# Optimization experiments

Measured on AMD Instinct MI355X. Metric: run time of the kernel, lower is better.

Reference implementation:

```python
import jax, jax.numpy as jnp
import numpy as np


def setup_inputs() -> dict:
    key = jax.random.key(0)
    k1, k2 = jax.random.split(key)
    f = jax.random.normal(k1, (4, 8192, 128), dtype=jnp.float32)
    f_ = jax.random.normal(k2, (4, 8192, 128), dtype=jnp.float32)
    return {"f": f, "f_": f_}


def reference(f, f_):
    # square_distance: [B,N,M] = |f|^2 + |f_|^2 - 2 f.f_
    # dis[b,n,m] = ||f[b,n] - f_[b,m]||^2
    dis = (jnp.sum(f * f, axis=-1)[:, :, None]
           + jnp.sum(f_ * f_, axis=-1)[:, None, :]
           - 2.0 * jnp.einsum('bnc,bmc->bnm', f, f_))
    f2f_ = jnp.min(dis, axis=2)   # [B, N]
    f_2f = jnp.min(dis, axis=1)   # [B, M]
    d = jnp.mean(f2f_, axis=1) + jnp.mean(f_2f, axis=1)  # [B]
    return jnp.mean(d)
```

## Files before the change

kernel.cpp:

```cpp
#include <hip/hip_runtime.h>

#define BATCH 4
#define NPTS 8192
#define DIM 128
#define TOTAL_ROWS (BATCH * NPTS)
#define SLICES 8
#define SLICE_W 1024
#define ITERS 64
#define TILES_PER_B 512
#define TILE_B 2048

typedef __attribute__((ext_vector_type(8))) int   i32x8;
typedef __attribute__((ext_vector_type(4))) float f32x4;

__device__ __forceinline__ unsigned encf(float f) {
  unsigned b = __float_as_uint(f);
  return b ^ ((unsigned)((int)b >> 31) | 0x80000000u);
}
__device__ __forceinline__ float decf(unsigned u) {
  unsigned b = (u & 0x80000000u) ? (u ^ 0x80000000u) : ~u;
  return __uint_as_float(b);
}

__device__ __forceinline__ void pk8(const float4& x, const float4& y,
                                    unsigned& lo, unsigned& hi) {
  lo = __builtin_amdgcn_cvt_pk_fp8_f32(x.x, x.y, 0, 0);
  lo = __builtin_amdgcn_cvt_pk_fp8_f32(x.z, x.w, lo, 1);
  hi = __builtin_amdgcn_cvt_pk_fp8_f32(y.x, y.y, 0, 0);
  hi = __builtin_amdgcn_cvt_pk_fp8_f32(y.z, y.w, hi, 1);
}

__global__ void pack_kernel(const float* __restrict__ f,
                            const float* __restrict__ f_,
                            unsigned char* __restrict__ pkA,
                            unsigned char* __restrict__ pkB,
                            float* __restrict__ fnh,
                            float* __restrict__ gnh,
                            unsigned int* __restrict__ rowmin,
                            unsigned int* __restrict__ colmin) {
  __shared__ float sred[16][17];
  int gb  = blockIdx.x;
  int tl  = threadIdx.x;
  if (tl < 8)        rowmin[gb * 8 + tl]       = 0xFFFFFFFFu;
  else if (tl < 16)  colmin[gb * 8 + (tl - 8)] = 0xFFFFFFFFu;

  const int isA = gb >> 11;
  const float* in = isA ? f : f_;
  unsigned char* pk = isA ? pkA : pkB;
  float* n2h = isA ? fnh : gnh;

  int fl  = tl >> 2;
  int p   = tl & 3;
  int row = fl & 15, kch = fl >> 4;
  int tile = gb & 2047;
  int b = tile >> 9, mtg = tile & 511;
  const float* src = in + (size_t)(b * NPTS + mtg * 16 + row) * DIM + kch * 32 + p * 8;
  float4 x = ((const float4*)src)[0], y = ((const float4*)src)[1];
  unsigned lo, hi;
  pk8(x, y, lo, hi);
  *(uint2*)(pk + (size_t)tile * TILE_B + fl * 32 + p * 8) = make_uint2(lo, hi);
  float s = 0.f;
  s = fmaf(x.x, x.x, s); s = fmaf(x.y, x.y, s);
  s = fmaf(x.z, x.z, s); s = fmaf(x.w, x.w, s);
  s = fmaf(y.x, y.x, s); s = fmaf(y.y, y.y, s);
  s = fmaf(y.z, y.z, s); s = fmaf(y.w, y.w, s);
  sred[row][kch * 4 + p] = s;
  __syncthreads();
  if (tl < 16) {
    float t = 0.f;
    #pragma unroll
    for (int j = 0; j < 16; ++j) t += sred[tl][j];
    n2h[tile * 16 + tl] = -0.5f * t;
  }
}

__global__ __launch_bounds__(256, 4)
void chamfer_mfma_kernel(const unsigned char* __restrict__ pkA,
                         const unsigned char* __restrict__ pkB,
                         const float* __restrict__ fnh,
                         const float* __restrict__ gnh,
                         unsigned int* __restrict__ rowmin,
                         unsigned int* __restrict__ colmin) {
  const int lane = threadIdx.x & 63;
  const int l15  = lane & 15;
  const int q    = lane >> 4;
  const int widx = threadIdx.x >> 6;
  const int loff = lane * 32;

  const int bid   = blockIdx.x;
  const int combo = (bid & 7) * 4 + ((bid >> 3) & 3);
  const int b     = combo >> 3;
  const int slice = combo & 7;
  const int rgrp  = bid >> 5;
  const int r0    = rgrp * 256 + widx * 64;
  const int bN    = b * NPTS;
  const int tile0 = b * TILES_PER_B + slice * ITERS;

  __shared__ unsigned cl[SLICE_W];
  #pragma unroll
  for (int k = 0; k < SLICE_W / 256; ++k)
    cl[threadIdx.x + k * 256] = 0xFFFFFFFFu;
  __syncthreads();

  i32x8 af[4];
  const int atile0 = b * TILES_PER_B + (r0 >> 4);
  #pragma unroll
  for (int t = 0; t < 4; ++t) {
    const unsigned char* ub = pkA + (size_t)(atile0 + t) * TILE_B;
    af[t] = *(const i32x8*)(ub + loff);
  }
  f32x4 h[4];
  #pragma unroll
  for (int t = 0; t < 4; ++t)
    #pragma unroll
    for (int i = 0; i < 4; ++i)
      h[t][i] = fnh[bN + r0 + t * 16 + q * 4 + i];

  float rowmax[4][4];
  #pragma unroll
  for (int t = 0; t < 4; ++t)
    #pragma unroll
    for (int i = 0; i < 4; ++i) rowmax[t][i] = -3.4e38f;

  const unsigned char* pkw = pkB + (size_t)tile0 * TILE_B;
  const float*         gnb = gnh + bN + slice * SLICE_W;

  auto loadB = [&](int mt, i32x8& bf, float& gv) {
    const unsigned char* ub = pkw + (size_t)mt * TILE_B;
    bf = *(const i32x8*)(ub + loff);
    gv = gnb[mt * 16 + l15];
  };

  auto compute = [&](const i32x8& bf, float g2, int mt) {
    f32x4 acc[4];
    __builtin_amdgcn_s_setprio(1);
    #pragma unroll
    for (int t = 0; t < 4; ++t)
      acc[t] = __builtin_amdgcn_mfma_scale_f32_16x16x128_f8f6f4(
          af[t], bf, h[t], 0, 0, 0, 0x7f7f7f7f, 0, 0x7f7f7f7f);
    __builtin_amdgcn_s_setprio(0);

    #pragma unroll
    for (int t = 0; t < 4; ++t)
      #pragma unroll
      for (int i = 0; i < 4; ++i)
        rowmax[t][i] = fmaxf(rowmax[t][i], acc[t][i] + g2);

    float m0 = fmaxf(fmaxf(acc[0][0], acc[0][1]), acc[0][2]);
    float m1 = fmaxf(fmaxf(acc[0][3], acc[1][0]), acc[1][1]);
    float m2 = fmaxf(fmaxf(acc[1][2], acc[1][3]), acc[2][0]);
    float m3 = fmaxf(fmaxf(acc[2][1], acc[2][2]), acc[2][3]);
    float m4 = fmaxf(fmaxf(acc[3][0], acc[3][1]), acc[3][2]);
    float n0 = fmaxf(fmaxf(m0, m1), m2);
    float n1 = fmaxf(fmaxf(m3, m4), acc[3][3]);
    float cmax = fmaxf(n0, n1);
    atomicMin(&cl[mt * 16 + l15], encf(-2.f * cmax));
  };

  i32x8 bA, bB;
  float gA, gB;
  loadB(0, bA, gA);
  for (int mt = 0; mt < ITERS; mt += 2) {
    loadB(mt + 1, bB, gB);
    compute(bA, gA, mt);
    loadB((mt + 2) & (ITERS - 1), bA, gA);
    compute(bB, gB, mt + 1);
  }

  #pragma unroll
  for (int t = 0; t < 4; ++t)
    #pragma unroll
    for (int i = 0; i < 4; ++i) {
      float v = rowmax[t][i];
      v = fmaxf(v, __shfl_xor(v, 1));
      v = fmaxf(v, __shfl_xor(v, 2));
      v = fmaxf(v, __shfl_xor(v, 4));
      v = fmaxf(v, __shfl_xor(v, 8));
      if (l15 == 0)
        atomicMin(&rowmin[bN + r0 + t * 16 + q * 4 + i], encf(-2.f * v));
    }

  __syncthreads();
  #pragma unroll
  for (int k = 0; k < SLICE_W / 256; ++k) {
    int c = threadIdx.x + k * 256;
    float d = decf(cl[c]) - 2.f * gnb[c];
    atomicMin(&colmin[bN + slice * SLICE_W + c], encf(d));
  }
}

__global__ void reduce_kernel(const unsigned int* __restrict__ rowmin,
                              const unsigned int* __restrict__ colmin,
                              float* __restrict__ out) {
  __shared__ float sbuf[16];
  float s = 0.f;
  for (int i = threadIdx.x; i < TOTAL_ROWS; i += 1024)
    s += decf(rowmin[i]) + decf(colmin[i]);
  #pragma unroll
  for (int o = 32; o >= 1; o >>= 1) s += __shfl_xor(s, o);
  if ((threadIdx.x & 63) == 0) sbuf[threadIdx.x >> 6] = s;
  __syncthreads();
  if (threadIdx.x == 0) {
    float t = 0.f;
    #pragma unroll
    for (int j = 0; j < 16; ++j) t += sbuf[j];
    out[0] = t / (float)TOTAL_ROWS;
  }
}

extern "C" void kernel_launch(void* const* d_in, const int* in_sizes, int n_in,
                              void* d_out, int out_size, void* d_ws, size_t ws_size,
                              hipStream_t stream) {
  (void)in_sizes; (void)n_in; (void)out_size; (void)ws_size;
  const float* f  = (const float*)d_in[0];
  const float* f_ = (const float*)d_in[1];

  char* ws = (char*)d_ws;
  unsigned char* pkB = (unsigned char*)ws;
  unsigned char* pkA = (unsigned char*)(ws + 4u * 1024u * 1024u);
  float* gnh = (float*)(ws + 8u * 1024u * 1024u);
  float* fnh = gnh + TOTAL_ROWS;
  unsigned int* rowmin = (unsigned int*)(fnh + TOTAL_ROWS);
  unsigned int* colmin = rowmin + TOTAL_ROWS;

  pack_kernel<<<4096, 256, 0, stream>>>(f, f_, pkA, pkB, fnh, gnh, rowmin, colmin);
  chamfer_mfma_kernel<<<1024, 256, 0, stream>>>(pkA, pkB, fnh, gnh, rowmin, colmin);
  reduce_kernel<<<1, 1024, 0, stream>>>(rowmin, colmin, (float*)d_out);
}
```

Baseline: 60.43 us.

## Deepen B-tile prefetch and pair MFMA groups before a shared epilogue

The main loop now keeps four B tiles in flight instead of two. It issues two tiles' worth of MFMAs back to back before running a combined epilogue, so matrix work can overlap with the max reductions and loads. The column bias is now added before the column max, so the final column write is a plain atomicMin with no decode and re-encode. The setprio hints are dropped and launch bounds are lowered from 4 to 3 waves per SIMD to leave room for the extra registers, which may reduce occupancy.

```diff
diff --git a/kernel.cpp b/kernel.cpp
--- a/kernel.cpp
+++ b/kernel.cpp
@@ -74,7 +74,7 @@
   }
 }
 
-__global__ __launch_bounds__(256, 4)
+__global__ __launch_bounds__(256, 3)
 void chamfer_mfma_kernel(const unsigned char* __restrict__ pkA,
                          const unsigned char* __restrict__ pkB,
                          const float* __restrict__ fnh,
@@ -131,40 +131,60 @@
     gv = gnb[mt * 16 + l15];
   };
 
-  auto compute = [&](const i32x8& bf, float g2, int mt) {
-    f32x4 acc[4];
-    __builtin_amdgcn_s_setprio(1);
+  auto mfma4 = [&](const i32x8& bf, f32x4 acc[4]) {
     #pragma unroll
     for (int t = 0; t < 4; ++t)
       acc[t] = __builtin_amdgcn_mfma_scale_f32_16x16x128_f8f6f4(
           af[t], bf, h[t], 0, 0, 0, 0x7f7f7f7f, 0, 0x7f7f7f7f);
-    __builtin_amdgcn_s_setprio(0);
-
+  };
+
+  auto epi2 = [&](const f32x4 a1[4], float ga, int mta,
+                  const f32x4 a2[4], float gb, int mtb) {
+    float e1[16], e2[16];
     #pragma unroll
     for (int t = 0; t < 4; ++t)
       #pragma unroll
-      for (int i = 0; i < 4; ++i)
-        rowmax[t][i] = fmaxf(rowmax[t][i], acc[t][i] + g2);
-
-    float m0 = fmaxf(fmaxf(acc[0][0], acc[0][1]), acc[0][2]);
-    float m1 = fmaxf(fmaxf(acc[0][3], acc[1][0]), acc[1][1]);
-    float m2 = fmaxf(fmaxf(acc[1][2], acc[1][3]), acc[2][0]);
-    float m3 = fmaxf(fmaxf(acc[2][1], acc[2][2]), acc[2][3]);
-    float m4 = fmaxf(fmaxf(acc[3][0], acc[3][1]), acc[3][2]);
+      for (int i = 0; i < 4; ++i) {
+        float x1 = a1[t][i] + ga;
+        float x2 = a2[t][i] + gb;
+        e1[t * 4 + i] = x1;
+        e2[t * 4 + i] = x2;
+        rowmax[t][i] = fmaxf(fmaxf(rowmax[t][i], x1), x2);
+      }
+    float m0 = fmaxf(fmaxf(e1[0], e1[1]), e1[2]);
+    float m1 = fmaxf(fmaxf(e1[3], e1[4]), e1[5]);
+    float m2 = fmaxf(fmaxf(e1[6], e1[7]), e1[8]);
+    float m3 = fmaxf(fmaxf(e1[9], e1[10]), e1[11]);
+    float m4 = fmaxf(fmaxf(e1[12], e1[13]), e1[14]);
     float n0 = fmaxf(fmaxf(m0, m1), m2);
-    float n1 = fmaxf(fmaxf(m3, m4), acc[3][3]);
-    float cmax = fmaxf(n0, n1);
-    atomicMin(&cl[mt * 16 + l15], encf(-2.f * cmax));
+    float n1 = fmaxf(fmaxf(m3, m4), e1[15]);
+    float c1 = fmaxf(n0, n1);
+    atomicMin(&cl[mta * 16 + l15], encf(-2.f * c1));
+    float p0 = fmaxf(fmaxf(e2[0], e2[1]), e2[2]);
+    float p1 = fmaxf(fmaxf(e2[3], e2[4]), e2[5]);
+    float p2 = fmaxf(fmaxf(e2[6], e2[7]), e2[8]);
+    float p3 = fmaxf(fmaxf(e2[9], e2[10]), e2[11]);
+    float p4 = fmaxf(fmaxf(e2[12], e2[13]), e2[14]);
+    float q0 = fmaxf(fmaxf(p0, p1), p2);
+    float q1 = fmaxf(fmaxf(p3, p4), e2[15]);
+    float c2 = fmaxf(q0, q1);
+    atomicMin(&cl[mtb * 16 + l15], encf(-2.f * c2));
   };
 
-  i32x8 bA, bB;
-  float gA, gB;
-  loadB(0, bA, gA);
-  for (int mt = 0; mt < ITERS; mt += 2) {
-    loadB(mt + 1, bB, gB);
-    compute(bA, gA, mt);
-    loadB((mt + 2) & (ITERS - 1), bA, gA);
-    compute(bB, gB, mt + 1);
+  i32x8 b0, b1, b2, b3;
+  float g0, g1, g2v, g3;
+  loadB(0, b0, g0); loadB(1, b1, g1); loadB(2, b2, g2v); loadB(3, b3, g3);
+  f32x4 acc1[4], acc2[4];
+  #pragma unroll 2
+  for (int mt = 0; mt < ITERS; mt += 4) {
+    mfma4(b0, acc1); mfma4(b1, acc2);
+    epi2(acc1, g0, mt, acc2, g1, mt + 1);
+    loadB((mt + 4) & (ITERS - 1), b0, g0);
+    loadB((mt + 5) & (ITERS - 1), b1, g1);
+    mfma4(b2, acc1); mfma4(b3, acc2);
+    epi2(acc1, g2v, mt + 2, acc2, g3, mt + 3);
+    loadB((mt + 6) & (ITERS - 1), b2, g2v);
+    loadB((mt + 7) & (ITERS - 1), b3, g3);
   }
 
   #pragma unroll
@@ -184,8 +204,7 @@
   #pragma unroll
   for (int k = 0; k < SLICE_W / 256; ++k) {
     int c = threadIdx.x + k * 256;
-    float d = decf(cl[c]) - 2.f * gnb[c];
-    atomicMin(&colmin[bN + slice * SLICE_W + c], encf(d));
+    atomicMin(&colmin[bN + slice * SLICE_W + c], cl[c]);
   }
 }
 
```

Result: faster. 57.79 us (-4.4%).
